# Performance work log

Measured on AMD Instinct MI355X. Metric: run time of the kernel, lower is better.

## Reference

```python
import jax, jax.numpy as jnp
import numpy as np

B, T, D, K = 8, 4096, 1024, 3


def setup_inputs() -> dict:
    key = jax.random.key(0)
    k0, k1, k2 = jax.random.split(key, 3)
    x = jax.random.normal(k0, (B, T, D), dtype=jnp.float32)
    lim = 1.0 / np.sqrt(D)
    Wv = jax.random.uniform(k1, (D, D), dtype=jnp.float32, minval=-lim, maxval=lim)
    bv = jnp.zeros((D,), dtype=jnp.float32)
    Wo = jax.random.uniform(k2, (D, D), dtype=jnp.float32, minval=-lim, maxval=lim)
    bo = jnp.zeros((D,), dtype=jnp.float32)
    neighbor_weights = jnp.ones((K,), dtype=jnp.float32) / K
    return {"x": x, "Wv": Wv, "bv": bv, "Wo": Wo, "bo": bo,
            "neighbor_weights": neighbor_weights}


def reference(x, Wv, bv, Wo, bo, neighbor_weights):
    # x: [B, T, D]; faithful translation of the unfold -> Linear -> weighted-sum chain
    k = neighbor_weights.shape[0]
    pad = k // 2
    t = x.shape[1]
    # replicate padding along T (torch F.pad mode='replicate')
    xp = jnp.pad(x, ((0, 0), (pad, pad), (0, 0)), mode='edge')  # [B, T+2*pad, D]
    # sliding windows: [B, T, K, D] (small fixed K loop, not a data-dim loop)
    windows = jnp.stack([xp[:, i:i + t, :] for i in range(k)], axis=2)
    # value projection applied per window element (nn.Linear: x @ W.T + b)
    v = jnp.einsum('btkd,ed->btke', windows, Wv) + bv  # [B, T, K, D]
    # fixed-weight neighbor average
    attended = jnp.einsum('btkd,k->btd', v, neighbor_weights)  # [B, T, D]
    # output projection
    return jnp.einsum('btd,ed->bte', attended, Wo) + bo
```

## Files before the change

kernel.cpp:

```cpp
#include <hip/hip_runtime.h>
#include <stdint.h>
#include <stddef.h>

typedef _Float16 f16_t;
typedef _Float16 f16x4 __attribute__((ext_vector_type(4)));
typedef _Float16 f16x8 __attribute__((ext_vector_type(8)));
typedef float f32x4 __attribute__((ext_vector_type(4)));

#define AS_G __attribute__((address_space(1)))
#define AS_L __attribute__((address_space(3)))

__device__ __forceinline__ void gload_lds16(const void* g, void* l) {
  __builtin_amdgcn_global_load_lds((AS_G void*)g, (AS_L void*)l, 16, 0, 0);
}

#define FENCE() asm volatile("" ::: "memory")
#define BARX()                            \
  do {                                    \
    FENCE();                              \
    __builtin_amdgcn_s_barrier();         \
    FENCE();                              \
  } while (0)
#define VMCNT(n) asm volatile("s_waitcnt vmcnt(" #n ")" ::: "memory")


__global__ __launch_bounds__(256) void prep_xavg_kernel(
    const float* __restrict__ X, const float* __restrict__ Wo,
    const float* __restrict__ Wv, const float* __restrict__ bv,
    const float* __restrict__ bo, const float* __restrict__ nw, int Kw,
    f16_t* __restrict__ Wo_h, f16_t* __restrict__ WvT, float* __restrict__ bc,
    f16_t* __restrict__ Xavg) {
  __shared__ float smem[32 * 33];
  const int b = blockIdx.x;
  const int t = threadIdx.x;
  if (b >= 3072) {
    const int T = 4096, D = 1024;
    const int base = (b - 3072) * 8;
    const int t0 = base & (T - 1);
    const int col = t * 4;
    const float w0 = nw[0], w1 = nw[1], w2 = nw[2];
    const float* xb = X + (size_t)base * D + col;
    f32x4 va = *(const f32x4*)(xb + (t0 == 0 ? 0 : -D));
    f32x4 vb = *(const f32x4*)(xb);
    f16_t* ob = Xavg + (size_t)base * D + col;
#pragma unroll
    for (int g = 0; g < 8; ++g) {
      f32x4 vc;
      if (t0 + g == T - 1) vc = vb;
      else vc = *(const f32x4*)(xb + (size_t)(g + 1) * D);
      f32x4 y = w0 * va + w1 * vb + w2 * vc;
      f16x4 o;
      o.x = (f16_t)y.x; o.y = (f16_t)y.y; o.z = (f16_t)y.z; o.w = (f16_t)y.w;
      *(f16x4*)(ob + (size_t)g * D) = o;
      va = vb;
      vb = vc;
    }
  } else if (b < 1024) {
    const int i = b * 256 + t;
    f32x4 v = ((const f32x4*)Wo)[i];
    f16x4 o;
    o.x = (f16_t)v.x; o.y = (f16_t)v.y; o.z = (f16_t)v.z; o.w = (f16_t)v.w;
    ((f16x4*)Wo_h)[i] = o;
  } else if (b < 2048) {
    const int i = b - 1024;
    const int bx = i & 31, by = i >> 5;
    const int tx = t & 31, ty = t >> 5;
#pragma unroll
    for (int k = 0; k < 32; k += 8)
      smem[(ty + k) * 33 + tx] = Wv[(size_t)(by * 32 + ty + k) * 1024 + bx * 32 + tx];
    __syncthreads();
#pragma unroll
    for (int k = 0; k < 32; k += 8)
      WvT[(size_t)(bx * 32 + ty + k) * 1024 + by * 32 + tx] = (f16_t)smem[tx * 33 + ty + k];
  } else {
    const int e = b - 2048;
    float sw = 0.f;
    for (int k = 0; k < Kw; ++k) sw += nw[k];
    float p = 0.f;
    for (int d = t; d < 1024; d += 256) p += Wo[(size_t)e * 1024 + d] * bv[d];
    smem[t] = p;
    __syncthreads();
    for (int s = 128; s > 0; s >>= 1) {
      if (t < s) smem[t] += smem[t + s];
      __syncthreads();
    }
    if (t == 0) bc[e] = sw * smem[0] + bo[e];
  }
}


template <typename OutT, bool BIAS>
__global__ __launch_bounds__(256) void gemm_bt_kernel(const f16_t* __restrict__ A,
                                                      const f16_t* __restrict__ Bt,
                                                      OutT* __restrict__ C,
                                                      const float* __restrict__ bias,
                                                      int M, int N, int K) {
  __shared__ __align__(16) f16_t sA[128 * 32];
  __shared__ __align__(16) f16_t sB[128 * 32];
  const int tid = threadIdx.x;
  const int l = tid & 63;
  const int w = tid >> 6;
  const int wr = w >> 1;
  const int wc = w & 1;
  const int nMT = M >> 7;
  const int bid = blockIdx.x;
  const int mt = bid % nMT;
  const int nt = bid / nMT;
  const int m0 = mt << 7;
  const int n0 = nt << 7;

  const int srow = (w << 4) + (l >> 2);
  const int scol = (l & 3) << 3;
  const size_t aoff0 = (size_t)(m0 + srow) * K + scol;
  const size_t boff0 = (size_t)(n0 + srow) * K + scol;
  f16_t* ldsA = sA + (w << 9);
  f16_t* ldsB = sB + (w << 9);

  f32x4 acc[4][4];
#pragma unroll
  for (int i = 0; i < 4; ++i)
#pragma unroll
    for (int j = 0; j < 4; ++j) acc[i][j] = f32x4{0.f, 0.f, 0.f, 0.f};

  const int ka = (l >> 4) << 3;
  const int ar = (wr << 6) + (l & 15);
  const int br = (wc << 6) + (l & 15);

  const int nK = K >> 5;
  for (int kt = 0; kt < nK; ++kt) {
    const int kb = kt << 5;
    gload_lds16(A + aoff0 + kb, ldsA);
    gload_lds16(A + aoff0 + ((size_t)K << 6) + kb, ldsA + 2048);
    gload_lds16(Bt + boff0 + kb, ldsB);
    gload_lds16(Bt + boff0 + ((size_t)K << 6) + kb, ldsB + 2048);
    __syncthreads();
    f16x8 af[4], bfr[4];
#pragma unroll
    for (int m = 0; m < 4; ++m) af[m] = *(const f16x8*)(sA + ((ar + (m << 4)) << 5) + ka);
#pragma unroll
    for (int n = 0; n < 4; ++n) bfr[n] = *(const f16x8*)(sB + ((br + (n << 4)) << 5) + ka);
#pragma unroll
    for (int m = 0; m < 4; ++m)
#pragma unroll
      for (int n = 0; n < 4; ++n)
        acc[m][n] = __builtin_amdgcn_mfma_f32_16x16x32_f16(af[m], bfr[n], acc[m][n], 0, 0, 0);
    __syncthreads();
  }

  const int orow = (l >> 4) << 2;
  const int ocol = l & 15;
#pragma unroll
  for (int n = 0; n < 4; ++n) {
    const int gn = n0 + (wc << 6) + (n << 4) + ocol;
    const float bs = BIAS ? bias[gn] : 0.f;
#pragma unroll
    for (int m = 0; m < 4; ++m) {
      const int gm = m0 + (wr << 6) + (m << 4) + orow;
#pragma unroll
      for (int j = 0; j < 4; ++j) {
        C[(size_t)(gm + j) * N + gn] = (OutT)(acc[m][n][j] + bs);
      }
    }
  }
}


__device__ __forceinline__ void stage256(const f16_t* __restrict__ g, int K,
                                         f16_t* ldsOp, int w, int l) {
#pragma unroll
  for (int i = 0; i < 2; ++i) {
    const int f = i * 512 + w * 64 + l;
    const int row = f >> 2;
    const int ch = f & 3;
    const int col = ((ch ^ ((row >> 1) & 3)) << 3);
    gload_lds16(g + (size_t)row * K + col, ldsOp + i * 4096 + w * 512);
  }
}

__global__ __launch_bounds__(512, 2) void gemm256_kernel(const f16_t* __restrict__ A,
                                                         const f16_t* __restrict__ Bt,
                                                         float* __restrict__ C,
                                                         const float* __restrict__ bias,
                                                         int M, int N, int K) {
  __shared__ __align__(16) f16_t lds[4 * 16384];
  const int tid = threadIdx.x;
  const int l = tid & 63;
  const int w = tid >> 6;
  const int wr = w >> 2;
  const int wc = w & 3;
  const int lr = l & 15;
  const int q = l >> 4;

  const int cpx = (int)gridDim.x >> 3;
  const int swzb = ((int)blockIdx.x & 7) * cpx + ((int)blockIdx.x >> 3);
  const int nNT = N >> 8;
  const int mt = swzb / nNT;
  const int nt = swzb % nNT;
  const int m0 = mt << 8;
  const int n0 = nt << 8;

  const f16_t* Apanel = A + (size_t)m0 * K;
  const f16_t* Bpanel = Bt + (size_t)n0 * K;
  const int sw = (q ^ ((lr >> 1) & 3)) << 3;

  f32x4 acc[8][4];
#pragma unroll
  for (int m = 0; m < 8; ++m)
#pragma unroll
    for (int n = 0; n < 4; ++n) acc[m][n] = f32x4{0.f, 0.f, 0.f, 0.f};

  const int nK = K >> 5;

  for (int t = 0; t < 3; ++t) {
    f16_t* buf = lds + (t & 3) * 16384;
    stage256(Apanel + (t << 5), K, buf, w, l);
    stage256(Bpanel + (t << 5), K, buf + 8192, w, l);
  }
  VMCNT(8);
  BARX();

  for (int t = 0; t < nK; ++t) {
    f16_t* sA = lds + (t & 3) * 16384;
    f16_t* sB = sA + 8192;

    {
      const int tn = (t + 3) < nK ? (t + 3) : (nK - 1);
      f16_t* nbuf = lds + ((t + 3) & 3) * 16384;
      stage256(Apanel + ((size_t)tn << 5), K, nbuf, w, l);
      stage256(Bpanel + ((size_t)tn << 5), K, nbuf + 8192, w, l);
    }

    f16x8 bf[4], af[4], ag[4];
#pragma unroll
    for (int n = 0; n < 4; ++n)
      bf[n] = *(const f16x8*)(sB + (((wc << 6) + (n << 4) + lr) << 5) + sw);
#pragma unroll
    for (int m = 0; m < 4; ++m)
      af[m] = *(const f16x8*)(sA + (((wr << 7) + (m << 4) + lr) << 5) + sw);
#pragma unroll
    for (int m = 0; m < 4; ++m)
      ag[m] = *(const f16x8*)(sA + (((wr << 7) + 64 + (m << 4) + lr) << 5) + sw);

    __builtin_amdgcn_s_setprio(1);
#pragma unroll
    for (int m = 0; m < 4; ++m)
#pragma unroll
      for (int n = 0; n < 4; ++n)
        acc[m][n] = __builtin_amdgcn_mfma_f32_16x16x32_f16(af[m], bf[n], acc[m][n], 0, 0, 0);
#pragma unroll
    for (int m = 0; m < 4; ++m)
#pragma unroll
      for (int n = 0; n < 4; ++n)
        acc[m + 4][n] = __builtin_amdgcn_mfma_f32_16x16x32_f16(ag[m], bf[n], acc[m + 4][n], 0, 0, 0);
    __builtin_amdgcn_s_setprio(0);

    VMCNT(8);
    BARX();
  }

  float bs[4];
#pragma unroll
  for (int n = 0; n < 4; ++n) bs[n] = bias[n0 + (wc << 6) + (n << 4) + lr];
#pragma unroll
  for (int m = 0; m < 8; ++m) {
    const int gm = m0 + (wr << 7) + (m << 4) + (q << 2);
#pragma unroll
    for (int j = 0; j < 4; ++j) {
      float* Crow = C + (size_t)(gm + j) * N + n0 + (wc << 6) + lr;
#pragma unroll
      for (int n = 0; n < 4; ++n) Crow[n << 4] = acc[m][n][j] + bs[n];
    }
  }
}


extern "C" void kernel_launch(void* const* d_in, const int* in_sizes, int n_in,
                              void* d_out, int out_size, void* d_ws, size_t ws_size,
                              hipStream_t stream) {
  const float* x = (const float*)d_in[0];
  const float* Wv = (const float*)d_in[1];
  const float* bv = (const float*)d_in[2];
  const float* Wo = (const float*)d_in[3];
  const float* bo = (const float*)d_in[4];
  const float* nw = (const float*)d_in[5];
  float* out = (float*)d_out;

  char* ws = (char*)d_ws;
  f16_t* Wo_h = (f16_t*)(ws);
  f16_t* WvT  = (f16_t*)(ws + (2u << 20));
  f16_t* WcT  = (f16_t*)(ws + (4u << 20));
  float* bc   = (float*)(ws + (6u << 20));
  f16_t* Xavg = (f16_t*)(ws + (8u << 20));

  prep_xavg_kernel<<<dim3(7168), dim3(256), 0, stream>>>(
      x, Wo, Wv, bv, bo, nw, in_sizes[5], Wo_h, WvT, bc, Xavg);
  gemm_bt_kernel<f16_t, false><<<dim3(64), dim3(256), 0, stream>>>(
      Wo_h, WvT, WcT, (const float*)nullptr, 1024, 1024, 1024);
  gemm256_kernel<<<dim3(512), dim3(512), 0, stream>>>(
      Xavg, WcT, out, bc, 32768, 1024, 1024);
}
```

Measured before the change: 146.8 us.

## Double-buffer LDS fragment reads in registers across K iterations

Unrolls the GEMM K loop by two and keeps two register sets of A/B fragments. The LDS reads for tile t+1 are issued before the MFMAs for tile t, so read latency overlaps with matrix math. The vmcnt wait tightens from 8 to 4 so tile t+1 is resident before it is read. This costs extra VGPRs for the second fragment set, which may hurt occupancy or cause spills. It also relies on nK being even.

Result: no change. 147.1 us (+0.2%).

```diff
diff --git a/kernel.cpp b/kernel.cpp
--- a/kernel.cpp
+++ b/kernel.cpp
@@ -216,47 +216,62 @@
     stage256(Apanel + (t << 5), K, buf, w, l);
     stage256(Bpanel + (t << 5), K, buf + 8192, w, l);
   }
-  VMCNT(8);
+  VMCNT(4);
   BARX();
 
-  for (int t = 0; t < nK; ++t) {
-    f16_t* sA = lds + (t & 3) * 16384;
-    f16_t* sB = sA + 8192;
-
-    {
-      const int tn = (t + 3) < nK ? (t + 3) : (nK - 1);
-      f16_t* nbuf = lds + ((t + 3) & 3) * 16384;
-      stage256(Apanel + ((size_t)tn << 5), K, nbuf, w, l);
-      stage256(Bpanel + ((size_t)tn << 5), K, nbuf + 8192, w, l);
-    }
-
-    f16x8 bf[4], af[4], ag[4];
-#pragma unroll
-    for (int n = 0; n < 4; ++n)
-      bf[n] = *(const f16x8*)(sB + (((wc << 6) + (n << 4) + lr) << 5) + sw);
-#pragma unroll
-    for (int m = 0; m < 4; ++m)
-      af[m] = *(const f16x8*)(sA + (((wr << 7) + (m << 4) + lr) << 5) + sw);
-#pragma unroll
-    for (int m = 0; m < 4; ++m)
-      ag[m] = *(const f16x8*)(sA + (((wr << 7) + 64 + (m << 4) + lr) << 5) + sw);
-
-    __builtin_amdgcn_s_setprio(1);
-#pragma unroll
-    for (int m = 0; m < 4; ++m)
-#pragma unroll
-      for (int n = 0; n < 4; ++n)
-        acc[m][n] = __builtin_amdgcn_mfma_f32_16x16x32_f16(af[m], bf[n], acc[m][n], 0, 0, 0);
-#pragma unroll
-    for (int m = 0; m < 4; ++m)
-#pragma unroll
-      for (int n = 0; n < 4; ++n)
-        acc[m + 4][n] = __builtin_amdgcn_mfma_f32_16x16x32_f16(ag[m], bf[n], acc[m + 4][n], 0, 0, 0);
-    __builtin_amdgcn_s_setprio(0);
-
-    VMCNT(8);
+  f16x8 af0[4], ag0[4], bf0[4], af1[4], ag1[4], bf1[4];
+
+#define READSET(SUF, GRAN)                                                        \
+  do {                                                                            \
+    const f16_t* gA_ = lds + (size_t)(GRAN) * 16384;                              \
+    const f16_t* gB_ = gA_ + 8192;                                                \
+    _Pragma("unroll") for (int n_ = 0; n_ < 4; ++n_)                              \
+      bf##SUF[n_] = *(const f16x8*)(gB_ + (((wc << 6) + (n_ << 4) + lr) << 5) + sw); \
+    _Pragma("unroll") for (int m_ = 0; m_ < 4; ++m_) {                            \
+      af##SUF[m_] = *(const f16x8*)(gA_ + (((wr << 7) + (m_ << 4) + lr) << 5) + sw); \
+      ag##SUF[m_] = *(const f16x8*)(gA_ + (((wr << 7) + 64 + (m_ << 4) + lr) << 5) + sw); \
+    }                                                                             \
+  } while (0)
+
+#define MFMASET(SUF)                                                              \
+  do {                                                                            \
+    __builtin_amdgcn_s_setprio(1);                                                \
+    _Pragma("unroll") for (int m_ = 0; m_ < 4; ++m_)                              \
+      _Pragma("unroll") for (int n_ = 0; n_ < 4; ++n_)                            \
+        acc[m_][n_] = __builtin_amdgcn_mfma_f32_16x16x32_f16(                     \
+            af##SUF[m_], bf##SUF[n_], acc[m_][n_], 0, 0, 0);                      \
+    _Pragma("unroll") for (int m_ = 0; m_ < 4; ++m_)                              \
+      _Pragma("unroll") for (int n_ = 0; n_ < 4; ++n_)                            \
+        acc[m_ + 4][n_] = __builtin_amdgcn_mfma_f32_16x16x32_f16(                 \
+            ag##SUF[m_], bf##SUF[n_], acc[m_ + 4][n_], 0, 0, 0);                  \
+    __builtin_amdgcn_s_setprio(0);                                                \
+  } while (0)
+
+#define STAGESTEP(TT)                                                             \
+  do {                                                                            \
+    const int tn_ = (TT) < nK ? (TT) : (nK - 1);                                  \
+    f16_t* g_ = lds + (tn_ & 3) * 16384;                                          \
+    stage256(Apanel + ((size_t)tn_ << 5), K, g_, w, l);                           \
+    stage256(Bpanel + ((size_t)tn_ << 5), K, g_ + 8192, w, l);                    \
+  } while (0)
+
+  READSET(0, 0);
+
+  for (int t = 0; t < nK; t += 2) {
+    STAGESTEP(t + 3);
+    READSET(1, (t + 1) & 3);
+    MFMASET(0);
+    VMCNT(4);
     BARX();
-  }
+    STAGESTEP(t + 4);
+    READSET(0, (t + 2) & 3);
+    MFMASET(1);
+    VMCNT(4);
+    BARX();
+  }
+#undef READSET
+#undef MFMASET
+#undef STAGESTEP
 
   float bs[4];
 #pragma unroll
```

## Restructure 256x256 GEMM mainloop to double-buffered K=64 tiles with phased MFMA

Applied to the files above, without the earlier changes.

The GEMM mainloop moves from a 4-deep ring of K=32 stages to two LDS buffers each holding a K=64 tile. The LDS swizzle is widened to 8 chunks to match. Each iteration is split into four MFMA quadrants, separated by barriers, sched_barrier and lgkmcnt waits, with fragment loads interleaved in a ping-pong style schedule. The goal is fewer barriers per unit of K and better overlap of LDS reads with MFMA issue. The cost is shallower prefetch depth (one tile ahead, with a full vmcnt(0) wait every iteration) and more barriers within each iteration.

Measured after the change: 145.8 us. No clear change (-0.7%).

```diff
diff --git a/kernel.cpp b/kernel.cpp
--- a/kernel.cpp
+++ b/kernel.cpp
@@ -22,6 +22,12 @@
     FENCE();                              \
   } while (0)
 #define VMCNT(n) asm volatile("s_waitcnt vmcnt(" #n ")" ::: "memory")
+#define LGKM0() asm volatile("s_waitcnt lgkmcnt(0)" ::: "memory")
+#if defined(__HIP_DEVICE_COMPILE__)
+#define SCHEDB0() __builtin_amdgcn_sched_barrier(0)
+#else
+#define SCHEDB0()
+#endif
 
 
 __global__ __launch_bounds__(256) void prep_xavg_kernel(
@@ -165,15 +171,14 @@
 }
 
 
-__device__ __forceinline__ void stage256(const f16_t* __restrict__ g, int K,
-                                         f16_t* ldsOp, int w, int l) {
-#pragma unroll
-  for (int i = 0; i < 2; ++i) {
+__device__ __forceinline__ void stage64(const f16_t* __restrict__ g, int K,
+                                        f16_t* ldsOp, int w, int l) {
+#pragma unroll
+  for (int i = 0; i < 4; ++i) {
     const int f = i * 512 + w * 64 + l;
-    const int row = f >> 2;
-    const int ch = f & 3;
-    const int col = ((ch ^ ((row >> 1) & 3)) << 3);
-    gload_lds16(g + (size_t)row * K + col, ldsOp + i * 4096 + w * 512);
+    const int row = f >> 3;
+    const int ch = (f & 7) ^ (row & 7);
+    gload_lds16(g + (size_t)row * K + (ch << 3), ldsOp + i * 4096 + w * 512);
   }
 }
 
@@ -182,7 +187,7 @@
                                                          float* __restrict__ C,
                                                          const float* __restrict__ bias,
                                                          int M, int N, int K) {
-  __shared__ __align__(16) f16_t lds[4 * 16384];
+  __shared__ __align__(16) f16_t lds[2 * 32768];
   const int tid = threadIdx.x;
   const int l = tid & 63;
   const int w = tid >> 6;
@@ -201,7 +206,15 @@
 
   const f16_t* Apanel = A + (size_t)m0 * K;
   const f16_t* Bpanel = Bt + (size_t)n0 * K;
-  const int sw = (q ^ ((lr >> 1) & 3)) << 3;
+
+  const int s0 = q ^ (lr & 7);
+  const int s1 = (4 + q) ^ (lr & 7);
+  const int arow = (wr << 7) + lr;
+  const int brow = (wc << 6) + lr;
+  const int aoff0 = arow * 64 + s0 * 8;
+  const int aoff1 = arow * 64 + s1 * 8;
+  const int boff0 = 16384 + brow * 64 + s0 * 8;
+  const int boff1 = 16384 + brow * 64 + s1 * 8;
 
   f32x4 acc[8][4];
 #pragma unroll
@@ -209,52 +222,95 @@
 #pragma unroll
     for (int n = 0; n < 4; ++n) acc[m][n] = f32x4{0.f, 0.f, 0.f, 0.f};
 
-  const int nK = K >> 5;
-
-  for (int t = 0; t < 3; ++t) {
-    f16_t* buf = lds + (t & 3) * 16384;
-    stage256(Apanel + (t << 5), K, buf, w, l);
-    stage256(Bpanel + (t << 5), K, buf + 8192, w, l);
-  }
-  VMCNT(8);
+  const int NT = K >> 6;
+
+  stage64(Apanel, K, lds, w, l);
+  stage64(Bpanel, K, lds + 16384, w, l);
+  VMCNT(0);
   BARX();
 
-  for (int t = 0; t < nK; ++t) {
-    f16_t* sA = lds + (t & 3) * 16384;
-    f16_t* sB = sA + 8192;
-
-    {
-      const int tn = (t + 3) < nK ? (t + 3) : (nK - 1);
-      f16_t* nbuf = lds + ((t + 3) & 3) * 16384;
-      stage256(Apanel + ((size_t)tn << 5), K, nbuf, w, l);
-      stage256(Bpanel + ((size_t)tn << 5), K, nbuf + 8192, w, l);
-    }
-
-    f16x8 bf[4], af[4], ag[4];
-#pragma unroll
-    for (int n = 0; n < 4; ++n)
-      bf[n] = *(const f16x8*)(sB + (((wc << 6) + (n << 4) + lr) << 5) + sw);
-#pragma unroll
-    for (int m = 0; m < 4; ++m)
-      af[m] = *(const f16x8*)(sA + (((wr << 7) + (m << 4) + lr) << 5) + sw);
-#pragma unroll
-    for (int m = 0; m < 4; ++m)
-      ag[m] = *(const f16x8*)(sA + (((wr << 7) + 64 + (m << 4) + lr) << 5) + sw);
-
+  for (int tt = 0; tt < NT; ++tt) {
+    f16_t* cur = lds + (tt & 1) * 32768;
+    f16_t* nxt = lds + ((tt + 1) & 1) * 32768;
+
+    f16x8 a0[4][2], a1[4][2], b0[2][2], b1[2][2];
+
+    if (tt + 1 < NT) {
+      stage64(Apanel + ((size_t)(tt + 1) << 6), K, nxt, w, l);
+      stage64(Bpanel + ((size_t)(tt + 1) << 6), K, nxt + 16384, w, l);
+    }
+#pragma unroll
+    for (int m = 0; m < 4; ++m) {
+      a0[m][0] = *(const f16x8*)(cur + aoff0 + m * 1024);
+      a0[m][1] = *(const f16x8*)(cur + aoff1 + m * 1024);
+    }
+#pragma unroll
+    for (int n = 0; n < 2; ++n) {
+      b0[n][0] = *(const f16x8*)(cur + boff0 + n * 1024);
+      b0[n][1] = *(const f16x8*)(cur + boff1 + n * 1024);
+    }
+    BARX();
+    LGKM0();
+    SCHEDB0();
     __builtin_amdgcn_s_setprio(1);
 #pragma unroll
     for (int m = 0; m < 4; ++m)
 #pragma unroll
-      for (int n = 0; n < 4; ++n)
-        acc[m][n] = __builtin_amdgcn_mfma_f32_16x16x32_f16(af[m], bf[n], acc[m][n], 0, 0, 0);
-#pragma unroll
-    for (int m = 0; m < 4; ++m)
-#pragma unroll
-      for (int n = 0; n < 4; ++n)
-        acc[m + 4][n] = __builtin_amdgcn_mfma_f32_16x16x32_f16(ag[m], bf[n], acc[m + 4][n], 0, 0, 0);
+      for (int n = 0; n < 2; ++n) {
+        acc[m][n] = __builtin_amdgcn_mfma_f32_16x16x32_f16(a0[m][0], b0[n][0], acc[m][n], 0, 0, 0);
+        acc[m][n] = __builtin_amdgcn_mfma_f32_16x16x32_f16(a0[m][1], b0[n][1], acc[m][n], 0, 0, 0);
+      }
     __builtin_amdgcn_s_setprio(0);
-
-    VMCNT(8);
+    BARX();
+
+#pragma unroll
+    for (int n = 0; n < 2; ++n) {
+      b1[n][0] = *(const f16x8*)(cur + boff0 + (n + 2) * 1024);
+      b1[n][1] = *(const f16x8*)(cur + boff1 + (n + 2) * 1024);
+    }
+    BARX();
+    LGKM0();
+    SCHEDB0();
+    __builtin_amdgcn_s_setprio(1);
+#pragma unroll
+    for (int m = 0; m < 4; ++m)
+#pragma unroll
+      for (int n = 0; n < 2; ++n) {
+        acc[m][n + 2] = __builtin_amdgcn_mfma_f32_16x16x32_f16(a0[m][0], b1[n][0], acc[m][n + 2], 0, 0, 0);
+        acc[m][n + 2] = __builtin_amdgcn_mfma_f32_16x16x32_f16(a0[m][1], b1[n][1], acc[m][n + 2], 0, 0, 0);
+      }
+    __builtin_amdgcn_s_setprio(0);
+    BARX();
+
+#pragma unroll
+    for (int m = 0; m < 4; ++m) {
+      a1[m][0] = *(const f16x8*)(cur + aoff0 + 4096 + m * 1024);
+      a1[m][1] = *(const f16x8*)(cur + aoff1 + 4096 + m * 1024);
+    }
+    BARX();
+    LGKM0();
+    SCHEDB0();
+    __builtin_amdgcn_s_setprio(1);
+#pragma unroll
+    for (int m = 0; m < 4; ++m)
+#pragma unroll
+      for (int n = 0; n < 2; ++n) {
+        acc[m + 4][n] = __builtin_amdgcn_mfma_f32_16x16x32_f16(a1[m][0], b0[n][0], acc[m + 4][n], 0, 0, 0);
+        acc[m + 4][n] = __builtin_amdgcn_mfma_f32_16x16x32_f16(a1[m][1], b0[n][1], acc[m + 4][n], 0, 0, 0);
+      }
+    __builtin_amdgcn_s_setprio(0);
+    BARX();
+
+    __builtin_amdgcn_s_setprio(1);
+#pragma unroll
+    for (int m = 0; m < 4; ++m)
+#pragma unroll
+      for (int n = 0; n < 2; ++n) {
+        acc[m + 4][n + 2] = __builtin_amdgcn_mfma_f32_16x16x32_f16(a1[m][0], b1[n][0], acc[m + 4][n + 2], 0, 0, 0);
+        acc[m + 4][n + 2] = __builtin_amdgcn_mfma_f32_16x16x32_f16(a1[m][1], b1[n][1], acc[m + 4][n + 2], 0, 0, 0);
+      }
+    __builtin_amdgcn_s_setprio(0);
+    VMCNT(0);
     BARX();
   }
 
```

## Load A fragments directly from global into registers, stage only B via LDS

Applied to the files above, without the earlier changes.

The A operand is no longer staged through LDS. Each wave loads its own A fragments straight from global memory into registers, double-buffered across two k-steps, while only B goes through LDS with a 4-slot ring. This halves LDS usage and LDS read traffic per k-step and cuts LDS staging work. In exchange it raises register pressure with 16 f16x8 A registers, uses less coalesced per-row global loads for A, and makes the vmcnt accounting tighter.

Result: slower. 227.0 us (+54.6%).

```diff
diff --git a/kernel.cpp b/kernel.cpp
--- a/kernel.cpp
+++ b/kernel.cpp
@@ -165,15 +165,14 @@
 }
 
 
-__device__ __forceinline__ void stage256(const f16_t* __restrict__ g, int K,
-                                         f16_t* ldsOp, int w, int l) {
+__device__ __forceinline__ void stageB(const f16_t* __restrict__ g, int K,
+                                       f16_t* gran, int w, int l) {
 #pragma unroll
   for (int i = 0; i < 2; ++i) {
     const int f = i * 512 + w * 64 + l;
     const int row = f >> 2;
-    const int ch = f & 3;
-    const int col = ((ch ^ ((row >> 1) & 3)) << 3);
-    gload_lds16(g + (size_t)row * K + col, ldsOp + i * 4096 + w * 512);
+    const int ch = (f & 3) ^ ((row >> 1) & 3);
+    gload_lds16(g + (size_t)row * K + (ch << 3), gran + i * 4096 + w * 512);
   }
 }
 
@@ -182,7 +181,7 @@
                                                          float* __restrict__ C,
                                                          const float* __restrict__ bias,
                                                          int M, int N, int K) {
-  __shared__ __align__(16) f16_t lds[4 * 16384];
+  __shared__ __align__(16) f16_t lds[4 * 8192];
   const int tid = threadIdx.x;
   const int l = tid & 63;
   const int w = tid >> 6;
@@ -201,6 +200,7 @@
 
   const f16_t* Apanel = A + (size_t)m0 * K;
   const f16_t* Bpanel = Bt + (size_t)n0 * K;
+  const f16_t* pA = Apanel + (size_t)((wr << 7) + lr) * K + (q << 3);
   const int sw = (q ^ ((lr >> 1) & 3)) << 3;
 
   f32x4 acc[8][4];
@@ -211,52 +211,69 @@
 
   const int nK = K >> 5;
 
-  for (int t = 0; t < 3; ++t) {
-    f16_t* buf = lds + (t & 3) * 16384;
-    stage256(Apanel + (t << 5), K, buf, w, l);
-    stage256(Bpanel + (t << 5), K, buf + 8192, w, l);
-  }
-  VMCNT(8);
+#define ALOAD(DST, KT)                                                  \
+  do {                                                                  \
+    const int kk_ = (KT) < nK ? (KT) : (nK - 1);                        \
+    const f16_t* p_ = pA + ((size_t)kk_ << 5);                          \
+    _Pragma("unroll") for (int m_ = 0; m_ < 8; ++m_)                    \
+      DST[m_] = *(const f16x8*)(p_ + (size_t)(m_ << 4) * K);            \
+  } while (0)
+
+#define BREAD(BF, GRAN)                                                 \
+  do {                                                                  \
+    const f16_t* gB_ = lds + (size_t)(GRAN) * 8192;                     \
+    _Pragma("unroll") for (int n_ = 0; n_ < 4; ++n_)                    \
+      BF[n_] = *(const f16x8*)(gB_ + (((wc << 6) + (n_ << 4) + lr) << 5) + sw); \
+  } while (0)
+
+#define MFMAS(AF, BF)                                                   \
+  do {                                                                  \
+    __builtin_amdgcn_s_setprio(1);                                      \
+    _Pragma("unroll") for (int m_ = 0; m_ < 8; ++m_)                    \
+      _Pragma("unroll") for (int n_ = 0; n_ < 4; ++n_)                  \
+        acc[m_][n_] = __builtin_amdgcn_mfma_f32_16x16x32_f16(           \
+            AF[m_], BF[n_], acc[m_][n_], 0, 0, 0);                      \
+    __builtin_amdgcn_s_setprio(0);                                      \
+  } while (0)
+
+#define STAGEB(TT)                                                      \
+  do {                                                                  \
+    const int ts_ = (TT) < nK ? (TT) : (nK - 1);                        \
+    stageB(Bpanel + (ts_ << 5), K, lds + (ts_ & 3) * 8192, w, l);       \
+  } while (0)
+
+  f16x8 af0[8], af1[8];
+
+  stageB(Bpanel, K, lds, w, l);
+  stageB(Bpanel + 32, K, lds + 8192, w, l);
+  ALOAD(af0, 0);
+  VMCNT(0);
   BARX();
 
-  for (int t = 0; t < nK; ++t) {
-    f16_t* sA = lds + (t & 3) * 16384;
-    f16_t* sB = sA + 8192;
-
+  for (int t = 0; t < nK; t += 2) {
     {
-      const int tn = (t + 3) < nK ? (t + 3) : (nK - 1);
-      f16_t* nbuf = lds + ((t + 3) & 3) * 16384;
-      stage256(Apanel + ((size_t)tn << 5), K, nbuf, w, l);
-      stage256(Bpanel + ((size_t)tn << 5), K, nbuf + 8192, w, l);
-    }
-
-    f16x8 bf[4], af[4], ag[4];
-#pragma unroll
-    for (int n = 0; n < 4; ++n)
-      bf[n] = *(const f16x8*)(sB + (((wc << 6) + (n << 4) + lr) << 5) + sw);
-#pragma unroll
-    for (int m = 0; m < 4; ++m)
-      af[m] = *(const f16x8*)(sA + (((wr << 7) + (m << 4) + lr) << 5) + sw);
-#pragma unroll
-    for (int m = 0; m < 4; ++m)
-      ag[m] = *(const f16x8*)(sA + (((wr << 7) + 64 + (m << 4) + lr) << 5) + sw);
-
-    __builtin_amdgcn_s_setprio(1);
-#pragma unroll
-    for (int m = 0; m < 4; ++m)
-#pragma unroll
-      for (int n = 0; n < 4; ++n)
-        acc[m][n] = __builtin_amdgcn_mfma_f32_16x16x32_f16(af[m], bf[n], acc[m][n], 0, 0, 0);
-#pragma unroll
-    for (int m = 0; m < 4; ++m)
-#pragma unroll
-      for (int n = 0; n < 4; ++n)
-        acc[m + 4][n] = __builtin_amdgcn_mfma_f32_16x16x32_f16(ag[m], bf[n], acc[m + 4][n], 0, 0, 0);
-    __builtin_amdgcn_s_setprio(0);
-
-    VMCNT(8);
-    BARX();
-  }
+      f16x8 bf[4];
+      BREAD(bf, t & 3);
+      ALOAD(af1, t + 1);
+      STAGEB(t + 2);
+      MFMAS(af0, bf);
+      VMCNT(2);
+      BARX();
+    }
+    {
+      f16x8 bf[4];
+      BREAD(bf, (t + 1) & 3);
+      ALOAD(af0, t + 2);
+      STAGEB(t + 3);
+      MFMAS(af1, bf);
+      VMCNT(2);
+      BARX();
+    }
+  }
+#undef ALOAD
+#undef BREAD
+#undef MFMAS
+#undef STAGEB
 
   float bs[4];
 #pragma unroll
```
